# Performance work log

Measured on AMD Instinct MI355X. Metric: run time of the kernel, lower is better.

The kernel has to match this reference:

```python
import jax, jax.numpy as jnp
import numpy as np

LN_EPS = 1e-5
LOG_EPS = 1e-8

def _layernorm(x, w, b):
    mu = jnp.mean(x, axis=-1, keepdims=True)
    var = jnp.mean((x - mu) ** 2, axis=-1, keepdims=True)
    return (x - mu) * jax.lax.rsqrt(var + LN_EPS) * w + b


def setup_inputs() -> dict:
    key = jax.random.key(0)
    ks = jax.random.split(key, 8)
    B, T, D = 4, 4096, 1024
    x = jax.random.normal(ks[0], (B, T, D), dtype=jnp.float32)
    ln_w = jnp.ones((D,), jnp.float32)
    ln_b = jnp.zeros((D,), jnp.float32)
    # torch Linear stores weight as (out, in)
    Wf = jax.random.normal(ks[1], (D, D), jnp.float32) / np.sqrt(D)
    bf = jax.random.normal(ks[2], (D,), jnp.float32) * 0.02
    # module inits reach to zeros; use small random values for a non-trivial baseline
    Wr = jax.random.normal(ks[3], (D, D), jnp.float32) * 0.02
    br = jax.random.normal(ks[4], (D,), jnp.float32) * 0.02
    alpha_bias = jnp.array([3.0], jnp.float32) + jax.random.normal(ks[5], (1,), jnp.float32) * 0.1
    beta_scale = jnp.array([0.02], jnp.float32)
    return {"x": x, "ln_w": ln_w, "ln_b": ln_b, "Wf": Wf, "bf": bf,
            "Wr": Wr, "br": br, "alpha_bias": alpha_bias, "beta_scale": beta_scale}


def reference(x, ln_w, ln_b, Wf, bf, Wr, br, alpha_bias, beta_scale):
    residual = x
    x_norm = _layernorm(x, ln_w, ln_b)                       # [B,T,D]
    alpha = jax.nn.sigmoid(jnp.einsum('btd,ed->bte', x_norm, Wf) + bf + alpha_bias)
    beta_x = beta_scale * (1.0 - alpha) * x_norm
    log_alpha = jnp.log(alpha + LOG_EPS)
    log_alpha_cumsum = jnp.cumsum(log_alpha, axis=1)          # [B,T,D]
    m = jnp.max(log_alpha_cumsum, axis=1, keepdims=True)      # [B,1,D]
    scale = jnp.exp(log_alpha_cumsum - m)
    x_star = beta_x * scale
    s_star = jnp.cumsum(x_star, axis=1)
    output = s_star / (scale + LOG_EPS)
    x_gate = jnp.tanh(jnp.einsum('btd,ed->bte', output, Wr) + br)
    return x_gate * 0.05 + residual
```

## Files before the change

kernel.cpp:

```cpp
#include <hip/hip_runtime.h>

#define D_DIM 1024
#define B_DIM 4
#define T_DIM 4096
#define M_DIM (B_DIM * T_DIM)
#define CHUNK 32
#define NCHUNK (T_DIM / CHUNK)
#define NWAVE_C 16
#define SEG (NCHUNK / NWAVE_C)
#define NKT (D_DIM / 32)

typedef unsigned short u16;
typedef __attribute__((ext_vector_type(8))) __bf16 bf16x8;
typedef __attribute__((ext_vector_type(4))) float f32x4;

__device__ __forceinline__ float bf2f(u16 u) {
    union { unsigned int i; float f; } v;
    v.i = ((unsigned int)u) << 16;
    return v.f;
}
__device__ __forceinline__ u16 f2bf(float f) {
    union { float f; unsigned int i; } v;
    v.f = f;
    unsigned int u = v.i;
    unsigned int r = (u + 0x7fffu + ((u >> 16) & 1u)) >> 16;
    return (u16)r;
}
__device__ __forceinline__ float fast_tanh(float v) {
    float e = __expf(2.f * v);
    return 1.f - 2.f / (e + 1.f);
}

#define GLOAD16(g, l)                                                   \
    __builtin_amdgcn_global_load_lds(                                   \
        (const __attribute__((address_space(1))) void*)(g),             \
        (__attribute__((address_space(3))) void*)(l), 16, 0, 0)

#define BAR()                                      \
    do {                                           \
        asm volatile("" ::: "memory");             \
        __builtin_amdgcn_s_barrier();              \
        asm volatile("" ::: "memory");             \
    } while (0)

#define WAITVM(N) asm volatile("s_waitcnt vmcnt(" #N ")" ::: "memory")

__global__ __launch_bounds__(256) void ln_conv_kernel(const float* __restrict__ x,
                                                      const float* __restrict__ w,
                                                      const float* __restrict__ b,
                                                      u16* __restrict__ xn,
                                                      const float* __restrict__ Wf,
                                                      const float* __restrict__ Wr,
                                                      u16* __restrict__ da,
                                                      u16* __restrict__ db) {
    int tid = threadIdx.x;
    if (blockIdx.x < 2048) {
        int i = blockIdx.x * 256 + tid;
        const float* s = (i < 262144) ? Wf : Wr;
        u16* dp = (i < 262144) ? da : db;
        int j = i & 262143;
        float4 v = ((const float4*)s)[j];
        ushort4 o;
        o.x = f2bf(v.x); o.y = f2bf(v.y); o.z = f2bf(v.z); o.w = f2bf(v.w);
        ((ushort4*)dp)[j] = o;
        return;
    }
    int wv = tid >> 6, lane = tid & 63;
    int row = (blockIdx.x - 2048) * 4 + wv;
    const float4* xr = (const float4*)(x + (size_t)row * D_DIM);
    float4 xv[4];
    #pragma unroll
    for (int k = 0; k < 4; k++) xv[k] = xr[lane + 64 * k];
    float s = 0.f, s2 = 0.f;
    #pragma unroll
    for (int k = 0; k < 4; k++) {
        s  += xv[k].x + xv[k].y + xv[k].z + xv[k].w;
        s2 += xv[k].x * xv[k].x + xv[k].y * xv[k].y
            + xv[k].z * xv[k].z + xv[k].w * xv[k].w;
    }
    #pragma unroll
    for (int o = 1; o < 64; o <<= 1) {
        s  += __shfl_xor(s, o, 64);
        s2 += __shfl_xor(s2, o, 64);
    }
    float mu = s * (1.0f / D_DIM);
    float var = s2 * (1.0f / D_DIM) - mu * mu;
    float rs = rsqrtf(var + 1e-5f);
    ushort4* xo = (ushort4*)(xn + (size_t)row * D_DIM);
    #pragma unroll
    for (int k = 0; k < 4; k++) {
        float4 wv4 = ((const float4*)w)[lane + 64 * k];
        float4 bv4 = ((const float4*)b)[lane + 64 * k];
        ushort4 o;
        o.x = f2bf((xv[k].x - mu) * rs * wv4.x + bv4.x);
        o.y = f2bf((xv[k].y - mu) * rs * wv4.y + bv4.y);
        o.z = f2bf((xv[k].z - mu) * rs * wv4.z + bv4.z);
        o.w = f2bf((xv[k].w - mu) * rs * wv4.w + bv4.w);
        xo[lane + 64 * k] = o;
    }
}

__device__ __forceinline__ void gemm256_core(const u16* __restrict__ AG,
                                             const u16* __restrict__ BG,
                                             int tile_m, int tile_n,
                                             u16* ldsA,
                                             f32x4 (*acc)[4]) {
    int tid  = threadIdx.x;
    int wave = tid >> 6, lane = tid & 63;
    int wr = wave >> 2, wc = wave & 3;
    int lrow = lane >> 2;
    int sswz = (lane & 3) ^ (lrow & 3);
    const u16* gA = AG + (size_t)(tile_m + wave * 32 + lrow) * D_DIM + sswz * 8;
    int ldst = wave * 1024 + lane * 8;
    int fr = lane & 15, q = lane >> 4;
    int sw = (q ^ (lane & 3)) * 8;
    const u16* pAb = ldsA + (wr * 128 + fr) * 32 + sw;
    const u16* pBF[4];
    #pragma unroll
    for (int ni = 0; ni < 4; ni++)
        pBF[ni] = BG + (size_t)(tile_n + wc * 64 + ni * 16 + fr) * D_DIM + q * 8;

#define STGA(tt)                                                             \
    do {                                                                     \
        GLOAD16(gA + (size_t)(tt) * 32,                                      \
                ldsA + ((tt) & 3) * 8192 + ldst);                            \
        GLOAD16(gA + (size_t)(tt) * 32 + (size_t)16 * D_DIM,                 \
                ldsA + ((tt) & 3) * 8192 + 512 + ldst);                      \
    } while (0)

    STGA(0); STGA(1); STGA(2);
    bf16x8 Bcur[4], Bnxt[4];
    #pragma unroll
    for (int ni = 0; ni < 4; ni++) Bcur[ni] = *(const bf16x8*)(pBF[ni]);
    WAITVM(8);
    BAR();

    for (int t = 0; t < NKT; t++) {
        if (t + 1 < NKT) {
            #pragma unroll
            for (int ni = 0; ni < 4; ni++)
                Bnxt[ni] = *(const bf16x8*)(pBF[ni] + (size_t)(t + 1) * 32);
        }
        const u16* pA = pAb + (t & 3) * 8192;
        bf16x8 Af[8];
        #pragma unroll
        for (int mi = 0; mi < 8; mi++) Af[mi] = *(const bf16x8*)(pA + mi * 512);
        #pragma unroll
        for (int mi = 0; mi < 8; mi++)
            #pragma unroll
            for (int ni = 0; ni < 4; ni++)
                acc[mi][ni] = __builtin_amdgcn_mfma_f32_16x16x32_bf16(
                    Af[mi], Bcur[ni], acc[mi][ni], 0, 0, 0);
        #pragma unroll
        for (int ni = 0; ni < 4; ni++) Bcur[ni] = Bnxt[ni];
        if (t + 3 < NKT) {
            STGA(t + 3);
            WAITVM(12);
        } else {
            WAITVM(4);
        }
        BAR();
    }
#undef STGA
}

__global__ __launch_bounds__(512, 2) void gemm1_kernel(const u16* __restrict__ xn,
                                                       const u16* __restrict__ Wfc,
                                                       const float* __restrict__ bf_,
                                                       const float* __restrict__ ab,
                                                       const float* __restrict__ bs,
                                                       u16* __restrict__ out_la,
                                                       float* __restrict__ Sg,
                                                       float* __restrict__ Tg) {
    __shared__ __align__(16) u16 lds[65536];
    int flat = blockIdx.y * 4 + blockIdx.x;
    int xcd = flat & 7, p = flat >> 3;
    int tile_m = (xcd * 8 + (p >> 2)) * 256;
    int tile_n = (p & 3) * 256;
    f32x4 acc[8][4] = {};
    gemm256_core(xn, Wfc, tile_m, tile_n, lds, acc);

    int tid = threadIdx.x, wave = tid >> 6, lane = tid & 63;
    int wr = wave >> 2, wc = wave & 3;
    int q = lane >> 4, l = lane & 15;
    #pragma unroll
    for (int j = 0; j < 16; j++) {
        int xrow = wave * 32 + j * 2 + (lane >> 5);
        int xslot = (lane & 31) ^ (xrow & 3);
        GLOAD16(xn + (size_t)(tile_m + xrow) * D_DIM + tile_n + xslot * 8,
                lds + wave * 8192 + j * 512 + lane * 8);
    }
    WAITVM(0);
    BAR();

    float abv = ab[0], bsv = bs[0];
    #pragma unroll
    for (int ni = 0; ni < 4; ni++) {
        int col = tile_n + wc * 64 + ni * 16 + l;
        float bcol = bf_[col];
        #pragma unroll
        for (int ch = 0; ch < 4; ch++) {
            float lav[2][4], bxv[2][4];
            #pragma unroll
            for (int h = 0; h < 2; h++) {
                int mi = 2 * ch + h;
                #pragma unroll
                for (int r = 0; r < 4; r++) {
                    int rl = wr * 128 + mi * 16 + q * 4 + r;
                    int cl = wc * 64 + ni * 16 + l;
                    int row = tile_m + rl;
                    float z = acc[mi][ni][r] + bcol + abv;
                    float alpha = 1.f / (1.f + __expf(-z));
                    float la_ = __logf(alpha + 1e-8f);
                    float xv = bf2f(lds[rl * 256 + (((cl >> 3) ^ (rl & 3)) * 8) + (cl & 7)]);
                    lav[h][r] = la_;
                    bxv[h][r] = bsv * (1.f - alpha) * xv;
                    out_la[(size_t)row * D_DIM + col] = f2bf(la_);
                }
            }
            float s0 = lav[0][0] + lav[0][1] + lav[0][2] + lav[0][3];
            float s1 = lav[1][0] + lav[1][1] + lav[1][2] + lav[1][3];
            float x0 = s0, x1 = s1, y;
            y = __shfl_up(x0, 16, 64); if (q >= 1) x0 += y;
            y = __shfl_up(x0, 32, 64); if (q >= 2) x0 += y;
            y = __shfl_up(x1, 16, 64); if (q >= 1) x1 += y;
            y = __shfl_up(x1, 32, 64); if (q >= 2) x1 += y;
            float t0 = __shfl(x0, l + 48, 64);
            float t1 = __shfl(x1, l + 48, 64);
            float e0 = x0 - s0, e1 = x1 - s1;
            float pr = e0, Tp = 0.f;
            #pragma unroll
            for (int r = 0; r < 4; r++) { pr += lav[0][r]; Tp += bxv[0][r] * __expf(pr); }
            pr = t0 + e1;
            #pragma unroll
            for (int r = 0; r < 4; r++) { pr += lav[1][r]; Tp += bxv[1][r] * __expf(pr); }
            Tp += __shfl_xor(Tp, 16, 64);
            Tp += __shfl_xor(Tp, 32, 64);
            if (q == 0) {
                int cidx = ((tile_m + wr * 128) >> 5) + ch;
                Sg[(size_t)cidx * D_DIM + col] = t0 + t1;
                Tg[(size_t)cidx * D_DIM + col] = Tp;
            }
        }
    }
}

__global__ __launch_bounds__(1024) void scan_combine(const u16* __restrict__ la,
                                                     const float* __restrict__ S,
                                                     const float* __restrict__ Tb,
                                                     float* __restrict__ Of,
                                                     float* __restrict__ SSp) {
    __shared__ float lsS[NWAVE_C][64], lsW[NWAVE_C][64];
    int b = blockIdx.x >> 4;
    int dg = blockIdx.x & 15;
    int wave = threadIdx.x >> 6, lane = threadIdx.x & 63;
    int d = dg * 64 + lane;
    float m = bf2f(la[(size_t)(b * T_DIM) * D_DIM + d]);
    size_t base = ((size_t)b * NCHUNK) * D_DIM + d;
    int c0 = wave * SEG;

    float OfR[SEG], wR[SEG];
    float Or = 0.f, w = 0.f;
    #pragma unroll
    for (int j = 0; j < SEG; j++) {
        size_t ci = base + (size_t)(c0 + j) * D_DIM;
        OfR[j] = Or;
        wR[j]  = w;
        w  += __expf(Or) * Tb[ci];
        Or += S[ci];
    }
    lsS[wave][lane] = Or; lsW[wave][lane] = w;
    __syncthreads();

    float o = 0.f, s = 0.f, myO = 0.f, myS = 0.f;
    #pragma unroll
    for (int w2 = 0; w2 < NWAVE_C; w2++) {
        if (w2 == wave) { myO = o; myS = s; }
        s += __expf(o - m) * lsW[w2][lane];
        o += lsS[w2][lane];
    }

    float em = __expf(myO - m);
    #pragma unroll
    for (int j = 0; j < SEG; j++) {
        size_t ci = base + (size_t)(c0 + j) * D_DIM;
        Of[ci]  = myO + OfR[j] - m;
        SSp[ci] = myS + em * wR[j];
    }
}

__global__ __launch_bounds__(256) void scan_final(const u16* __restrict__ la,
                                                  const u16* __restrict__ xn,
                                                  const float* __restrict__ bs,
                                                  const float* __restrict__ Of,
                                                  const float* __restrict__ SSp,
                                                  u16* __restrict__ osc) {
    int bc = blockIdx.x;
    int b = bc >> 7, c = bc & (NCHUNK - 1);
    int col0 = threadIdx.x * 4;
    float bsv = bs[0];
    size_t base = ((size_t)(b * T_DIM + c * CHUNK)) * D_DIM + col0;
    size_t ci = ((size_t)(b * NCHUNK + c)) * D_DIM + col0;
    float ofs[4], ss[4], p[4];
    #pragma unroll
    for (int j = 0; j < 4; j++) { ofs[j] = Of[ci + j]; ss[j] = SSp[ci + j]; p[j] = 0.f; }
    #pragma unroll 8
    for (int t = 0; t < CHUNK; t++) {
        size_t idx = base + (size_t)t * D_DIM;
        ushort4 lv = *(const ushort4*)(la + idx);
        ushort4 xv = *(const ushort4*)(xn + idx);
        u16 lvs[4] = {lv.x, lv.y, lv.z, lv.w};
        u16 xvs[4] = {xv.x, xv.y, xv.z, xv.w};
        u16 os[4];
        #pragma unroll
        for (int j = 0; j < 4; j++) {
            float lav = bf2f(lvs[j]);
            p[j] += lav;
            float scv = __expf(ofs[j] + p[j]);
            float bx = bsv * (1.f - __expf(lav)) * bf2f(xvs[j]);
            ss[j] += bx * scv;
            os[j] = f2bf(ss[j] / (scv + 1e-8f));
        }
        ushort4 o; o.x = os[0]; o.y = os[1]; o.z = os[2]; o.w = os[3];
        *(ushort4*)(osc + idx) = o;
    }
}

__global__ __launch_bounds__(512, 2) void gemm2_kernel(const u16* __restrict__ A,
                                                       const u16* __restrict__ Bm,
                                                       const float* __restrict__ bias,
                                                       const float* __restrict__ resid,
                                                       float* __restrict__ out_f) {
    __shared__ __align__(16) u16 lds[32768];
    int flat = blockIdx.y * 4 + blockIdx.x;
    int xcd = flat & 7, p = flat >> 3;
    int tile_m = (xcd * 8 + (p >> 2)) * 256;
    int tile_n = (p & 3) * 256;
    f32x4 acc[8][4] = {};
    gemm256_core(A, Bm, tile_m, tile_n, lds, acc);

    int tid = threadIdx.x, wave = tid >> 6, lane = tid & 63;
    int wr = wave >> 2, wc = wave & 3;
    int q = lane >> 4, l = lane & 15;
    #pragma unroll
    for (int mi = 0; mi < 8; mi++) {
        #pragma unroll
        for (int r = 0; r < 4; r++) {
            int row = tile_m + wr * 128 + mi * 16 + q * 4 + r;
            #pragma unroll
            for (int ni = 0; ni < 4; ni++) {
                int col = tile_n + wc * 64 + ni * 16 + l;
                size_t idx = (size_t)row * D_DIM + col;
                float g = fast_tanh(acc[mi][ni][r] + bias[col]);
                out_f[idx] = 0.05f * g + resid[idx];
            }
        }
    }
}

extern "C" void kernel_launch(void* const* d_in, const int* in_sizes, int n_in,
                              void* d_out, int out_size, void* d_ws, size_t ws_size,
                              hipStream_t stream) {
    const float* x   = (const float*)d_in[0];
    const float* lnw = (const float*)d_in[1];
    const float* lnb = (const float*)d_in[2];
    const float* Wf  = (const float*)d_in[3];
    const float* bf_ = (const float*)d_in[4];
    const float* Wr  = (const float*)d_in[5];
    const float* br  = (const float*)d_in[6];
    const float* ab  = (const float*)d_in[7];
    const float* bs  = (const float*)d_in[8];
    float* out = (float*)d_out;

    char* w = (char*)d_ws;
    u16* xn  = (u16*)w;
    u16* la  = (u16*)(w + (size_t)33554432);
    u16* Wfc = (u16*)(w + (size_t)67108864);
    u16* Wrc = (u16*)(w + (size_t)69206016);
    float* S   = (float*)(w + (size_t)71303168);
    float* Tb  = S  + 524288;
    float* Of  = Tb + 524288;
    float* SSp = Of + 524288;
    u16* osc = xn;

    ln_conv_kernel<<<dim3(2048 + M_DIM / 4), dim3(256), 0, stream>>>(
        x, lnw, lnb, xn, Wf, Wr, Wfc, Wrc);
    gemm1_kernel<<<dim3(D_DIM / 256, M_DIM / 256), dim3(512), 0, stream>>>(
        xn, Wfc, bf_, ab, bs, la, S, Tb);
    scan_combine<<<dim3(B_DIM * 16), dim3(1024), 0, stream>>>(la, S, Tb, Of, SSp);
    scan_final<<<dim3(B_DIM * NCHUNK), dim3(256), 0, stream>>>(la, xn, bs, Of, SSp, osc);
    gemm2_kernel<<<dim3(D_DIM / 256, M_DIM / 256), dim3(512), 0, stream>>>(
        osc, Wrc, br, x, out);
}
```

Baseline: 283.2 us.

## Replace block-shared GEMM tiling with barrier-free per-wave 64x128 tiles

Rewrites the shared GEMM core so each wave owns a private 64x128 output tile with its own double-buffered LDS region for A. This removes block-wide barriers. B fragments are loaded straight from global memory each k-step, and the block tile becomes 512x128. The gemm1 epilogue drops its LDS staging of xn and reads xn directly from global memory. The cost is more global and L2 traffic for B, since the eight waves no longer share B data, and a shallower prefetch pipeline.

New measurement: 339.7 us. 1.2x slower.

```diff
diff --git a/kernel.cpp b/kernel.cpp
--- a/kernel.cpp
+++ b/kernel.cpp
@@ -36,14 +36,8 @@
         (const __attribute__((address_space(1))) void*)(g),             \
         (__attribute__((address_space(3))) void*)(l), 16, 0, 0)
 
-#define BAR()                                      \
-    do {                                           \
-        asm volatile("" ::: "memory");             \
-        __builtin_amdgcn_s_barrier();              \
-        asm volatile("" ::: "memory");             \
-    } while (0)
-
 #define WAITVM(N) asm volatile("s_waitcnt vmcnt(" #N ")" ::: "memory")
+#define WAITLGKM0() asm volatile("s_waitcnt lgkmcnt(0)" ::: "memory")
 
 __global__ __launch_bounds__(256) void ln_conv_kernel(const float* __restrict__ x,
                                                       const float* __restrict__ w,
@@ -100,66 +94,47 @@
     }
 }
 
-__device__ __forceinline__ void gemm256_core(const u16* __restrict__ AG,
-                                             const u16* __restrict__ BG,
-                                             int tile_m, int tile_n,
-                                             u16* ldsA,
-                                             f32x4 (*acc)[4]) {
-    int tid  = threadIdx.x;
-    int wave = tid >> 6, lane = tid & 63;
-    int wr = wave >> 2, wc = wave & 3;
-    int lrow = lane >> 2;
-    int sswz = (lane & 3) ^ (lrow & 3);
-    const u16* gA = AG + (size_t)(tile_m + wave * 32 + lrow) * D_DIM + sswz * 8;
-    int ldst = wave * 1024 + lane * 8;
+__device__ __forceinline__ void gemm_wave_core(const u16* __restrict__ AG,
+                                               const u16* __restrict__ BG,
+                                               int tile_m, int tile_n,
+                                               u16* ldsWave,
+                                               f32x4 (*acc)[8]) {
+    int lane = threadIdx.x & 63;
+    int wave = threadIdx.x >> 6;
     int fr = lane & 15, q = lane >> 4;
-    int sw = (q ^ (lane & 3)) * 8;
-    const u16* pAb = ldsA + (wr * 128 + fr) * 32 + sw;
-    const u16* pBF[4];
-    #pragma unroll
-    for (int ni = 0; ni < 4; ni++)
-        pBF[ni] = BG + (size_t)(tile_n + wc * 64 + ni * 16 + fr) * D_DIM + q * 8;
-
-#define STGA(tt)                                                             \
-    do {                                                                     \
-        GLOAD16(gA + (size_t)(tt) * 32,                                      \
-                ldsA + ((tt) & 3) * 8192 + ldst);                            \
-        GLOAD16(gA + (size_t)(tt) * 32 + (size_t)16 * D_DIM,                 \
-                ldsA + ((tt) & 3) * 8192 + 512 + ldst);                      \
+    int lr = lane >> 2;
+    const u16* gA = AG + (size_t)(tile_m + wave * 64 + lr) * D_DIM
+                  + (((lane & 3) ^ (lr & 3)) * 8);
+    const u16* pAb = ldsWave + fr * 32 + (q ^ (fr & 3)) * 8;
+    const u16* pB = BG + (size_t)(tile_n + fr) * D_DIM + q * 8;
+
+#define STGA(tt)                                                            \
+    do {                                                                    \
+        _Pragma("unroll") for (int j = 0; j < 4; j++)                       \
+            GLOAD16(gA + (size_t)j * (16 * D_DIM) + (size_t)(tt) * 32,      \
+                    ldsWave + ((tt) & 1) * 2048 + j * 512);                 \
     } while (0)
 
-    STGA(0); STGA(1); STGA(2);
-    bf16x8 Bcur[4], Bnxt[4];
-    #pragma unroll
-    for (int ni = 0; ni < 4; ni++) Bcur[ni] = *(const bf16x8*)(pBF[ni]);
-    WAITVM(8);
-    BAR();
-
+    STGA(0);
+    STGA(1);
     for (int t = 0; t < NKT; t++) {
-        if (t + 1 < NKT) {
-            #pragma unroll
-            for (int ni = 0; ni < 4; ni++)
-                Bnxt[ni] = *(const bf16x8*)(pBF[ni] + (size_t)(t + 1) * 32);
-        }
-        const u16* pA = pAb + (t & 3) * 8192;
-        bf16x8 Af[8];
-        #pragma unroll
-        for (int mi = 0; mi < 8; mi++) Af[mi] = *(const bf16x8*)(pA + mi * 512);
-        #pragma unroll
-        for (int mi = 0; mi < 8; mi++)
-            #pragma unroll
-            for (int ni = 0; ni < 4; ni++)
+        WAITVM(4);
+        bf16x8 Bf[8];
+        #pragma unroll
+        for (int ni = 0; ni < 8; ni++)
+            Bf[ni] = *(const bf16x8*)(pB + (size_t)ni * (16 * D_DIM) + (size_t)t * 32);
+        const u16* pA = pAb + (t & 1) * 2048;
+        bf16x8 Af[4];
+        #pragma unroll
+        for (int mi = 0; mi < 4; mi++) Af[mi] = *(const bf16x8*)(pA + mi * 512);
+        WAITLGKM0();
+        if (t + 2 < NKT) STGA(t + 2);
+        #pragma unroll
+        for (int mi = 0; mi < 4; mi++)
+            #pragma unroll
+            for (int ni = 0; ni < 8; ni++)
                 acc[mi][ni] = __builtin_amdgcn_mfma_f32_16x16x32_bf16(
-                    Af[mi], Bcur[ni], acc[mi][ni], 0, 0, 0);
-        #pragma unroll
-        for (int ni = 0; ni < 4; ni++) Bcur[ni] = Bnxt[ni];
-        if (t + 3 < NKT) {
-            STGA(t + 3);
-            WAITVM(12);
-        } else {
-            WAITVM(4);
-        }
-        BAR();
+                    Af[mi], Bf[ni], acc[mi][ni], 0, 0, 0);
     }
 #undef STGA
 }
@@ -172,47 +147,34 @@
                                                        u16* __restrict__ out_la,
                                                        float* __restrict__ Sg,
                                                        float* __restrict__ Tg) {
-    __shared__ __align__(16) u16 lds[65536];
-    int flat = blockIdx.y * 4 + blockIdx.x;
+    __shared__ __align__(16) u16 lds[32768];
+    int flat = blockIdx.y * 8 + blockIdx.x;
     int xcd = flat & 7, p = flat >> 3;
-    int tile_m = (xcd * 8 + (p >> 2)) * 256;
-    int tile_n = (p & 3) * 256;
-    f32x4 acc[8][4] = {};
-    gemm256_core(xn, Wfc, tile_m, tile_n, lds, acc);
-
-    int tid = threadIdx.x, wave = tid >> 6, lane = tid & 63;
-    int wr = wave >> 2, wc = wave & 3;
+    int tile_m = (xcd * 4 + (p & 3)) * 512;
+    int tile_n = (p >> 2) * 128;
+    int wave = threadIdx.x >> 6, lane = threadIdx.x & 63;
+    f32x4 acc[4][8] = {};
+    gemm_wave_core(xn, Wfc, tile_m, tile_n, lds + wave * 4096, acc);
+
+    float abv = ab[0], bsv = bs[0];
     int q = lane >> 4, l = lane & 15;
     #pragma unroll
-    for (int j = 0; j < 16; j++) {
-        int xrow = wave * 32 + j * 2 + (lane >> 5);
-        int xslot = (lane & 31) ^ (xrow & 3);
-        GLOAD16(xn + (size_t)(tile_m + xrow) * D_DIM + tile_n + xslot * 8,
-                lds + wave * 8192 + j * 512 + lane * 8);
-    }
-    WAITVM(0);
-    BAR();
-
-    float abv = ab[0], bsv = bs[0];
-    #pragma unroll
-    for (int ni = 0; ni < 4; ni++) {
-        int col = tile_n + wc * 64 + ni * 16 + l;
+    for (int ni = 0; ni < 8; ni++) {
+        int col = tile_n + ni * 16 + l;
         float bcol = bf_[col];
         #pragma unroll
-        for (int ch = 0; ch < 4; ch++) {
+        for (int ch = 0; ch < 2; ch++) {
             float lav[2][4], bxv[2][4];
             #pragma unroll
             for (int h = 0; h < 2; h++) {
                 int mi = 2 * ch + h;
                 #pragma unroll
                 for (int r = 0; r < 4; r++) {
-                    int rl = wr * 128 + mi * 16 + q * 4 + r;
-                    int cl = wc * 64 + ni * 16 + l;
-                    int row = tile_m + rl;
+                    int row = tile_m + wave * 64 + mi * 16 + q * 4 + r;
                     float z = acc[mi][ni][r] + bcol + abv;
                     float alpha = 1.f / (1.f + __expf(-z));
                     float la_ = __logf(alpha + 1e-8f);
-                    float xv = bf2f(lds[rl * 256 + (((cl >> 3) ^ (rl & 3)) * 8) + (cl & 7)]);
+                    float xv = bf2f(xn[(size_t)row * D_DIM + col]);
                     lav[h][r] = la_;
                     bxv[h][r] = bsv * (1.f - alpha) * xv;
                     out_la[(size_t)row * D_DIM + col] = f2bf(la_);
@@ -237,7 +199,7 @@
             Tp += __shfl_xor(Tp, 16, 64);
             Tp += __shfl_xor(Tp, 32, 64);
             if (q == 0) {
-                int cidx = ((tile_m + wr * 128) >> 5) + ch;
+                int cidx = ((tile_m + wave * 64) >> 5) + ch;
                 Sg[(size_t)cidx * D_DIM + col] = t0 + t1;
                 Tg[(size_t)cidx * D_DIM + col] = Tp;
             }
@@ -332,24 +294,23 @@
                                                        const float* __restrict__ resid,
                                                        float* __restrict__ out_f) {
     __shared__ __align__(16) u16 lds[32768];
-    int flat = blockIdx.y * 4 + blockIdx.x;
+    int flat = blockIdx.y * 8 + blockIdx.x;
     int xcd = flat & 7, p = flat >> 3;
-    int tile_m = (xcd * 8 + (p >> 2)) * 256;
-    int tile_n = (p & 3) * 256;
-    f32x4 acc[8][4] = {};
-    gemm256_core(A, Bm, tile_m, tile_n, lds, acc);
-
-    int tid = threadIdx.x, wave = tid >> 6, lane = tid & 63;
-    int wr = wave >> 2, wc = wave & 3;
+    int tile_m = (xcd * 4 + (p & 3)) * 512;
+    int tile_n = (p >> 2) * 128;
+    int wave = threadIdx.x >> 6, lane = threadIdx.x & 63;
+    f32x4 acc[4][8] = {};
+    gemm_wave_core(A, Bm, tile_m, tile_n, lds + wave * 4096, acc);
+
     int q = lane >> 4, l = lane & 15;
     #pragma unroll
-    for (int mi = 0; mi < 8; mi++) {
+    for (int mi = 0; mi < 4; mi++) {
         #pragma unroll
         for (int r = 0; r < 4; r++) {
-            int row = tile_m + wr * 128 + mi * 16 + q * 4 + r;
-            #pragma unroll
-            for (int ni = 0; ni < 4; ni++) {
-                int col = tile_n + wc * 64 + ni * 16 + l;
+            int row = tile_m + wave * 64 + mi * 16 + q * 4 + r;
+            #pragma unroll
+            for (int ni = 0; ni < 8; ni++) {
+                int col = tile_n + ni * 16 + l;
                 size_t idx = (size_t)row * D_DIM + col;
                 float g = fast_tanh(acc[mi][ni][r] + bias[col]);
                 out_f[idx] = 0.05f * g + resid[idx];
@@ -385,10 +346,10 @@
 
     ln_conv_kernel<<<dim3(2048 + M_DIM / 4), dim3(256), 0, stream>>>(
         x, lnw, lnb, xn, Wf, Wr, Wfc, Wrc);
-    gemm1_kernel<<<dim3(D_DIM / 256, M_DIM / 256), dim3(512), 0, stream>>>(
+    gemm1_kernel<<<dim3(D_DIM / 128, M_DIM / 512), dim3(512), 0, stream>>>(
         xn, Wfc, bf_, ab, bs, la, S, Tb);
     scan_combine<<<dim3(B_DIM * 16), dim3(1024), 0, stream>>>(la, S, Tb, Of, SSp);
     scan_final<<<dim3(B_DIM * NCHUNK), dim3(256), 0, stream>>>(la, xn, bs, Of, SSp, osc);
-    gemm2_kernel<<<dim3(D_DIM / 256, M_DIM / 256), dim3(512), 0, stream>>>(
+    gemm2_kernel<<<dim3(D_DIM / 128, M_DIM / 512), dim3(512), 0, stream>>>(
         osc, Wrc, br, x, out);
 }
```
